# Kernel tuning notes

Measured on AMD Instinct MI355X. Metric: run time of the kernel, lower is better.

The kernel has to match this reference:

```python
import jax, jax.numpy as jnp
import numpy as np

NUM_INPUTS = 24
FACTOR = 16
VOCAB = 1_000_000
BATCH = 8192
PAIRS = NUM_INPUTS * (NUM_INPUTS - 1) // 2  # 276
HIDDEN = 64


def setup_inputs() -> dict:
    key = jax.random.key(0)
    ks = jax.random.split(key, 8)
    inputs = jax.random.randint(ks[0], (BATCH, NUM_INPUTS), 0, VOCAB)
    s = 0.01
    w = jax.random.normal(ks[1], (VOCAB, 1), dtype=jnp.float32) * s
    v = jax.random.normal(ks[2], (VOCAB, FACTOR), dtype=jnp.float32) * s
    b = jnp.zeros((1,), dtype=jnp.float32)
    W1 = jax.random.normal(ks[3], (PAIRS, 2 * FACTOR, HIDDEN), dtype=jnp.float32) * s
    b1 = jnp.zeros((PAIRS, HIDDEN), dtype=jnp.float32)
    W2 = jax.random.normal(ks[4], (PAIRS, HIDDEN, 1), dtype=jnp.float32) * s
    b2 = jnp.zeros((PAIRS, 1), dtype=jnp.float32)
    return {"inputs": inputs, "w": w, "v": v, "b": b,
            "W1": W1, "b1": b1, "W2": W2, "b2": b2}


def reference(inputs, w, v, b, W1, b1, W2, b2):
    # pair index lists (i < j) -- static
    ii, jj = np.triu_indices(NUM_INPUTS, k=1)
    ii = jnp.asarray(ii)
    jj = jnp.asarray(jj)

    # linear term: sum of 1-dim embeddings over fields
    xw = w[inputs]                      # [B, n, 1]
    l = jnp.sum(xw, axis=(1, 2))        # [B]

    # pairwise concat of factor embeddings
    xv = v[inputs]                      # [B, n, f]
    prods = jnp.concatenate([xv[:, ii, :], xv[:, jj, :]], axis=-1)  # [B, P, 2f]
    prods = jnp.transpose(prods, (1, 0, 2))                         # [P, B, 2f]

    # per-pair stacked MLP: layer 0 relu, layer 1 identity
    h = jax.nn.relu(jnp.einsum('pbi,pio->pbo', prods, W1) + b1[:, None, :])  # [P, B, H]
    out = jnp.einsum('pbi,pio->pbo', h, W2) + b2[:, None, :]                  # [P, B, 1]

    # sum over concat of pair outputs == sum over pairs and last dim
    p = jnp.sum(out, axis=(0, 2))       # [B]

    logits = l + p + b[0]
    return jax.nn.sigmoid(logits)
```

## Files before the change

kernel.cpp:

```cpp
#include <hip/hip_runtime.h>
#include <hip/hip_bf16.h>
#include <math.h>

#define BATCH   8192
#define NFIELD  24
#define FAC     16
#define PAIRS   276
#define NSETS   24
#define SETLEN  12
#define NBB     (BATCH / 64)

typedef __attribute__((ext_vector_type(8))) __bf16 bf16x8;
typedef __attribute__((ext_vector_type(4))) float f32x4;

#define XVT_OFF   0
#define COMBO_OFF 6291456
#define PART_OFF  (COMBO_OFF + 1285632)
#define WVAL_OFF  (PART_OFF + 786432)
#define CONST_OFF (WVAL_OFF + 786432)

__global__ void prep_all(const int* __restrict__ inputs,
                         const float* __restrict__ v,
                         const float* __restrict__ w,
                         const float* __restrict__ W1,
                         const float* __restrict__ W2,
                         const float* __restrict__ b1,
                         const float* __restrict__ b2,
                         const float* __restrict__ bsc,
                         __hip_bfloat16* __restrict__ xvT,
                         char* __restrict__ combo,
                         float* __restrict__ wval,
                         float* __restrict__ consts) {
    __shared__ float red[256];
    int blk = blockIdx.x;
    if (blk < 768) {
        int t = blk * 256 + threadIdx.x;
        int field = t >> 13;
        int b = t & 8191;
        int idx = inputs[b * NFIELD + field];
        const float4* src = (const float4*)(v + (long)idx * FAC);
        union { __hip_bfloat16 h[16]; uint4 u[2]; } tmp;
        float4 a0 = src[0], a1 = src[1], a2 = src[2], a3 = src[3];
        tmp.h[0]  = __float2bfloat16(a0.x); tmp.h[1]  = __float2bfloat16(a0.y);
        tmp.h[2]  = __float2bfloat16(a0.z); tmp.h[3]  = __float2bfloat16(a0.w);
        tmp.h[4]  = __float2bfloat16(a1.x); tmp.h[5]  = __float2bfloat16(a1.y);
        tmp.h[6]  = __float2bfloat16(a1.z); tmp.h[7]  = __float2bfloat16(a1.w);
        tmp.h[8]  = __float2bfloat16(a2.x); tmp.h[9]  = __float2bfloat16(a2.y);
        tmp.h[10] = __float2bfloat16(a2.z); tmp.h[11] = __float2bfloat16(a2.w);
        tmp.h[12] = __float2bfloat16(a3.x); tmp.h[13] = __float2bfloat16(a3.y);
        tmp.h[14] = __float2bfloat16(a3.z); tmp.h[15] = __float2bfloat16(a3.w);
        int bb = b >> 6, row = b & 63;
        __hip_bfloat16* base = xvT + (long)bb * 24576 + field * 1024 + row * 8;
        *(uint4*)base         = tmp.u[0];
        *(uint4*)(base + 512) = tmp.u[1];
        wval[field * BATCH + b] = w[idx];
    } else {
        int wb = blk - 768;
        int t = wb * 256 + threadIdx.x;
        int p = t >> 6;
        int L = t & 63;
        int q = L >> 4, c = L & 15;
        char* base = combo + (long)p * 4608;
        union { __hip_bfloat16 h[8]; uint4 u; } buf;
#pragma unroll
        for (int tt = 0; tt < 4; ++tt) {
#pragma unroll
            for (int jj = 0; jj < 8; ++jj)
                buf.h[jj] = __float2bfloat16(W1[p * 2048 + (q * 8 + jj) * 64 + tt * 16 + c]);
            *(uint4*)(base + 512 + tt * 1024 + L * 16) = buf.u;
        }
        if (L < 16) {
            float4 bv = {b1[p * 64 + L], b1[p * 64 + 16 + L], b1[p * 64 + 32 + L], b1[p * 64 + 48 + L]};
            *(float4*)(base + L * 16) = bv;
            float4 wv = {W2[p * 64 + L], W2[p * 64 + 16 + L], W2[p * 64 + 32 + L], W2[p * 64 + 48 + L]};
            *(float4*)(base + 256 + L * 16) = wv;
        }
        if (wb == 1) {
            uint4 z = {0, 0, 0, 0};
            for (int k = threadIdx.x; k < 576; k += 256)
                *(uint4*)(combo + (long)PAIRS * 4608 + k * 16) = z;
        }
        if (wb == 0) {
            float s = 0.f;
            for (int k = threadIdx.x; k < PAIRS; k += 256) s += b2[k];
            red[threadIdx.x] = s;
            __syncthreads();
            for (int off = 128; off > 0; off >>= 1) {
                if (threadIdx.x < off) red[threadIdx.x] += red[threadIdx.x + off];
                __syncthreads();
            }
            if (threadIdx.x == 0) consts[0] = red[0] + bsc[0];
        }
    }
}

struct Pkg {
    f32x4 cb0, cb1, cb2, cb3;
    float4 mw;
    bf16x8 f0, f1, f2, f3;
};

__device__ __forceinline__ Pkg load_pkg(const char* p, int mcol, int l16) {
    Pkg k;
    float4 tb = *(const float4*)(p + mcol);
    k.cb0 = (f32x4){tb.x, tb.x, tb.x, tb.x};
    k.cb1 = (f32x4){tb.y, tb.y, tb.y, tb.y};
    k.cb2 = (f32x4){tb.z, tb.z, tb.z, tb.z};
    k.cb3 = (f32x4){tb.w, tb.w, tb.w, tb.w};
    k.mw = *(const float4*)(p + 256 + mcol);
    k.f0 = *(const bf16x8*)(p + 512  + l16);
    k.f1 = *(const bf16x8*)(p + 1536 + l16);
    k.f2 = *(const bf16x8*)(p + 2560 + l16);
    k.f3 = *(const bf16x8*)(p + 3584 + l16);
    return k;
}

#define PKGCOMP(P)                                                            \
    {                                                                         \
        int fso = ((quad < 2) ? i : j) * 1088;                                \
        const f32x4 z4 = {0.f, 0.f, 0.f, 0.f};                                \
        _Pragma("unroll")                                                     \
        for (int t = 0; t < 4; ++t) {                                         \
            bf16x8 af = *(const bf16x8*)(xv_s + fso + abase + t * 128);       \
            f32x4 c0 = __builtin_amdgcn_mfma_f32_16x16x32_bf16(af, P.f0, P.cb0, 0, 0, 0); \
            f32x4 c1 = __builtin_amdgcn_mfma_f32_16x16x32_bf16(af, P.f1, P.cb1, 0, 0, 0); \
            f32x4 c2 = __builtin_amdgcn_mfma_f32_16x16x32_bf16(af, P.f2, P.cb2, 0, 0, 0); \
            f32x4 c3 = __builtin_amdgcn_mfma_f32_16x16x32_bf16(af, P.f3, P.cb3, 0, 0, 0); \
            acc[t] = acc[t] + __builtin_elementwise_max(c0, z4) * P.mw.x;     \
            acc[t] = acc[t] + __builtin_elementwise_max(c1, z4) * P.mw.y;     \
            acc[t] = acc[t] + __builtin_elementwise_max(c2, z4) * P.mw.z;     \
            acc[t] = acc[t] + __builtin_elementwise_max(c3, z4) * P.mw.w;     \
        }                                                                     \
        ++j;                                                                  \
        if (j == NFIELD) { ++i; j = i + 1; }                                  \
    }

__global__ __launch_bounds__(256, 3) void ffm_main(
        const __hip_bfloat16* __restrict__ xvT,
        const char* __restrict__ combo,
        float* __restrict__ partial) {
    __shared__ __align__(16) __hip_bfloat16 xv_s[24 * 1088];

    int tid  = threadIdx.x;
    int bb   = blockIdx.x & (NBB - 1);
    int pg   = blockIdx.x >> 7;
    int lane = tid & 63;
    int wave = tid >> 6;
    int col  = lane & 15;
    int quad = lane >> 4;

    {
        const uint4* src = (const uint4*)(xvT + (long)bb * 24576);
#pragma unroll
        for (int it = 0; it < 12; ++it) {
            int ch = tid + it * 256;
            *(uint4*)(xv_s + ch * 8 + (ch >> 6) * 32) = src[ch];
        }
    }
    __syncthreads();

    int setid = pg * 4 + wave;
    f32x4 acc[4];
#pragma unroll
    for (int t = 0; t < 4; ++t) acc[t] = (f32x4){0.f, 0.f, 0.f, 0.f};

    const int abase = (quad & 1) * 544 + col * 8;
    const int mcol  = col * 16;
    const int l16   = lane * 16;

    if (setid < 23) {
        int p0 = setid * SETLEN;
        int i = 0, rem = p0;
        while (rem >= NFIELD - 1 - i) { rem -= NFIELD - 1 - i; ++i; }
        int j = i + 1 + rem;

        const char* wp = combo + (long)p0 * 4608;
        Pkg A = load_pkg(wp, mcol, l16);
        Pkg B = load_pkg(wp + 4608, mcol, l16);

#pragma unroll 2
        for (int k = 0; k < SETLEN; k += 2) {
            PKGCOMP(A)
            A = load_pkg(wp + 2 * 4608, mcol, l16);
            PKGCOMP(B)
            B = load_pkg(wp + 3 * 4608, mcol, l16);
            wp += 2 * 4608;
        }
    }

#pragma unroll
    for (int m = 1; m < 16; m <<= 1) {
#pragma unroll
        for (int t = 0; t < 4; ++t) {
#pragma unroll
            for (int r = 0; r < 4; ++r) acc[t][r] += __shfl_xor(acc[t][r], m, 64);
        }
    }
    if (col == 0) {
#pragma unroll
        for (int t = 0; t < 4; ++t) {
            f32x4 o = acc[t];
            *(f32x4*)&partial[setid * BATCH + bb * 64 + t * 16 + quad * 4] = o;
        }
    }
}

__global__ void finalize(const float* __restrict__ wval,
                         const float* __restrict__ consts,
                         const float* __restrict__ partial,
                         float* __restrict__ out) {
    int b = blockIdx.x * 256 + threadIdx.x;
    float s = consts[0];
#pragma unroll
    for (int f = 0; f < NFIELD; ++f) s += wval[f * BATCH + b];
#pragma unroll
    for (int g = 0; g < NSETS; ++g) s += partial[g * BATCH + b];
    out[b] = 1.0f / (1.0f + expf(-s));
}

extern "C" void kernel_launch(void* const* d_in, const int* in_sizes, int n_in,
                              void* d_out, int out_size, void* d_ws, size_t ws_size,
                              hipStream_t stream) {
    const int*   inputs = (const int*)d_in[0];
    const float* w      = (const float*)d_in[1];
    const float* v      = (const float*)d_in[2];
    const float* bsc    = (const float*)d_in[3];
    const float* W1     = (const float*)d_in[4];
    const float* b1     = (const float*)d_in[5];
    const float* W2     = (const float*)d_in[6];
    const float* b2     = (const float*)d_in[7];
    float* out = (float*)d_out;

    char* ws = (char*)d_ws;
    __hip_bfloat16* xvT = (__hip_bfloat16*)(ws + XVT_OFF);
    char*  combo   = ws + COMBO_OFF;
    float* partial = (float*)(ws + PART_OFF);
    float* wval    = (float*)(ws + WVAL_OFF);
    float* consts  = (float*)(ws + CONST_OFF);

    prep_all<<<768 + 69, 256, 0, stream>>>(inputs, v, w, W1, W2, b1, b2, bsc,
                                           xvT, combo, wval, consts);
    ffm_main<<<NBB * 6, 256, 0, stream>>>(xvT, combo, partial);
    finalize<<<BATCH / 256, 256, 0, stream>>>(wval, consts, partial, out);
}
```

Before: 137.1 us.

## Fuse embedding gather and bf16 conversion into main kernel, drop xvT staging buffer

Removes the prep stage that gathered factor embeddings, converted them to bf16 and wrote a transposed xvT buffer to global memory. Each ffm_main block now gathers its own 64 rows × 24 fields directly from v, converts them and writes into shared memory. The prep kernel shrinks to linear-term and weight-packing work. The intent is to avoid the 6 MB global round trip, but each batch tile is now re-gathered by the 6 pair-group blocks that share it, so random v reads are repeated 6 times.

```diff
diff --git a/kernel.cpp b/kernel.cpp
--- a/kernel.cpp
+++ b/kernel.cpp
@@ -13,49 +13,35 @@
 typedef __attribute__((ext_vector_type(8))) __bf16 bf16x8;
 typedef __attribute__((ext_vector_type(4))) float f32x4;
 
-#define XVT_OFF   0
-#define COMBO_OFF 6291456
-#define PART_OFF  (COMBO_OFF + 1285632)
+#define COMBO_OFF 0
+#define PART_OFF  1281024
 #define WVAL_OFF  (PART_OFF + 786432)
 #define CONST_OFF (WVAL_OFF + 786432)
 
-__global__ void prep_all(const int* __restrict__ inputs,
-                         const float* __restrict__ v,
-                         const float* __restrict__ w,
-                         const float* __restrict__ W1,
-                         const float* __restrict__ W2,
-                         const float* __restrict__ b1,
-                         const float* __restrict__ b2,
-                         const float* __restrict__ bsc,
-                         __hip_bfloat16* __restrict__ xvT,
-                         char* __restrict__ combo,
-                         float* __restrict__ wval,
-                         float* __restrict__ consts) {
+__global__ void prep_small(const int* __restrict__ inputs,
+                           const float* __restrict__ w,
+                           const float* __restrict__ W1,
+                           const float* __restrict__ W2,
+                           const float* __restrict__ b1,
+                           const float* __restrict__ b2,
+                           const float* __restrict__ bsc,
+                           char* __restrict__ combo,
+                           float* __restrict__ wval,
+                           float* __restrict__ consts) {
     __shared__ float red[256];
     int blk = blockIdx.x;
-    if (blk < 768) {
+    if (blk < 96) {
         int t = blk * 256 + threadIdx.x;
-        int field = t >> 13;
-        int b = t & 8191;
-        int idx = inputs[b * NFIELD + field];
-        const float4* src = (const float4*)(v + (long)idx * FAC);
-        union { __hip_bfloat16 h[16]; uint4 u[2]; } tmp;
-        float4 a0 = src[0], a1 = src[1], a2 = src[2], a3 = src[3];
-        tmp.h[0]  = __float2bfloat16(a0.x); tmp.h[1]  = __float2bfloat16(a0.y);
-        tmp.h[2]  = __float2bfloat16(a0.z); tmp.h[3]  = __float2bfloat16(a0.w);
-        tmp.h[4]  = __float2bfloat16(a1.x); tmp.h[5]  = __float2bfloat16(a1.y);
-        tmp.h[6]  = __float2bfloat16(a1.z); tmp.h[7]  = __float2bfloat16(a1.w);
-        tmp.h[8]  = __float2bfloat16(a2.x); tmp.h[9]  = __float2bfloat16(a2.y);
-        tmp.h[10] = __float2bfloat16(a2.z); tmp.h[11] = __float2bfloat16(a2.w);
-        tmp.h[12] = __float2bfloat16(a3.x); tmp.h[13] = __float2bfloat16(a3.y);
-        tmp.h[14] = __float2bfloat16(a3.z); tmp.h[15] = __float2bfloat16(a3.w);
-        int bb = b >> 6, row = b & 63;
-        __hip_bfloat16* base = xvT + (long)bb * 24576 + field * 1024 + row * 8;
-        *(uint4*)base         = tmp.u[0];
-        *(uint4*)(base + 512) = tmp.u[1];
-        wval[field * BATCH + b] = w[idx];
+#pragma unroll
+        for (int k = 0; k < 8; ++k) {
+            int u = t + k * 24576;
+            int field = u >> 13;
+            int b = u & 8191;
+            int idx = inputs[b * NFIELD + field];
+            wval[field * BATCH + b] = w[idx];
+        }
     } else {
-        int wb = blk - 768;
+        int wb = blk - 96;
         int t = wb * 256 + threadIdx.x;
         int p = t >> 6;
         int L = t & 63;
@@ -136,7 +122,8 @@
     }
 
 __global__ __launch_bounds__(256, 3) void ffm_main(
-        const __hip_bfloat16* __restrict__ xvT,
+        const int* __restrict__ inputs,
+        const float* __restrict__ v,
         const char* __restrict__ combo,
         float* __restrict__ partial) {
     __shared__ __align__(16) __hip_bfloat16 xv_s[24 * 1088];
@@ -150,11 +137,27 @@
     int quad = lane >> 4;
 
     {
-        const uint4* src = (const uint4*)(xvT + (long)bb * 24576);
-#pragma unroll
-        for (int it = 0; it < 12; ++it) {
-            int ch = tid + it * 256;
-            *(uint4*)(xv_s + ch * 8 + (ch >> 6) * 32) = src[ch];
+        int row0 = bb * 64;
+#pragma unroll
+        for (int u6 = 0; u6 < 6; ++u6) {
+            int u = tid + u6 * 256;
+            int field = u >> 6;
+            int row = u & 63;
+            int idx = inputs[(row0 + row) * NFIELD + field];
+            const float4* src = (const float4*)(v + (long)idx * FAC);
+            float4 a0 = src[0], a1 = src[1], a2 = src[2], a3 = src[3];
+            union { __hip_bfloat16 h[8]; uint4 q; } lo, hi;
+            lo.h[0] = __float2bfloat16(a0.x); lo.h[1] = __float2bfloat16(a0.y);
+            lo.h[2] = __float2bfloat16(a0.z); lo.h[3] = __float2bfloat16(a0.w);
+            lo.h[4] = __float2bfloat16(a1.x); lo.h[5] = __float2bfloat16(a1.y);
+            lo.h[6] = __float2bfloat16(a1.z); lo.h[7] = __float2bfloat16(a1.w);
+            hi.h[0] = __float2bfloat16(a2.x); hi.h[1] = __float2bfloat16(a2.y);
+            hi.h[2] = __float2bfloat16(a2.z); hi.h[3] = __float2bfloat16(a2.w);
+            hi.h[4] = __float2bfloat16(a3.x); hi.h[5] = __float2bfloat16(a3.y);
+            hi.h[6] = __float2bfloat16(a3.z); hi.h[7] = __float2bfloat16(a3.w);
+            __hip_bfloat16* base = xv_s + field * 1088 + row * 8;
+            *(uint4*)base         = lo.q;
+            *(uint4*)(base + 544) = hi.q;
         }
     }
     __syncthreads();
@@ -232,14 +235,13 @@
     float* out = (float*)d_out;
 
     char* ws = (char*)d_ws;
-    __hip_bfloat16* xvT = (__hip_bfloat16*)(ws + XVT_OFF);
     char*  combo   = ws + COMBO_OFF;
     float* partial = (float*)(ws + PART_OFF);
     float* wval    = (float*)(ws + WVAL_OFF);
     float* consts  = (float*)(ws + CONST_OFF);
 
-    prep_all<<<768 + 69, 256, 0, stream>>>(inputs, v, w, W1, W2, b1, b2, bsc,
-                                           xvT, combo, wval, consts);
-    ffm_main<<<NBB * 6, 256, 0, stream>>>(xvT, combo, partial);
+    prep_small<<<165, 256, 0, stream>>>(inputs, w, W1, W2, b1, b2, bsc,
+                                        combo, wval, consts);
+    ffm_main<<<NBB * 6, 256, 0, stream>>>(inputs, v, combo, partial);
     finalize<<<BATCH / 256, 256, 0, stream>>>(wval, consts, partial, out);
 }
```

Measured after the change: 139.3 us. No clear change (+1.6%).
